# Optimization experiments

Measured on AMD Instinct MI355X. Metric: run time of the kernel, lower is better.

The kernel has to match this reference:

```python
import jax, jax.numpy as jnp
import numpy as np


def setup_inputs() -> dict:
    key = jax.random.key(0)
    ks = jax.random.split(key, 5)
    S, B, I, H = 512, 64, 256, 1024
    scale_x = 1.0 / np.sqrt(I)
    scale_h = 1.0 / np.sqrt(H)
    return {
        "x": jax.random.normal(ks[0], (S, B, I), dtype=jnp.float32),
        "Wx": jax.random.normal(ks[1], (H, I), dtype=jnp.float32) * scale_x,
        "bx": jax.random.normal(ks[2], (H,), dtype=jnp.float32) * scale_x,
        "Wh": jax.random.normal(ks[3], (H, H), dtype=jnp.float32) * scale_h,
        "bh": jax.random.normal(ks[4], (H,), dtype=jnp.float32) * scale_h,
    }


def reference(x, Wx, bx, Wh, bh):
    # x: (S, B, I). Vanilla RNN: h_t = tanh(Wh h_{t-1} + bh + Wx x_t + bx)
    S, B, I = x.shape
    H = Wh.shape[0]
    # Precompute input projections for all timesteps in one big GEMM.
    xproj = jnp.einsum("sbi,hi->sbh", x, Wx) + bx  # (S, B, H)

    def step(h, xp_t):
        h_new = jnp.tanh(h @ Wh.T + bh + xp_t)  # (B, H)
        return h_new, h_new

    h0 = jnp.zeros((B, H), dtype=x.dtype)
    h_last, h_seq = jax.lax.scan(step, h0, xproj)
    return h_seq, h_last[None]  # (S,B,H), (1,B,H)
```

## Files before the change

### kernel.cpp

```cpp
#include <hip/hip_runtime.h>
#include <cstddef>

#define S_ 512
#define B_ 64
#define I_ 256
#define H_ 1024

#define NG 8
#define GB 8
#define JT 32
#define GBLK 32

__global__ __launch_bounds__(256) void transpose_k(const float* __restrict__ in,
                                                   float* __restrict__ out,
                                                   int R, int C) {
  __shared__ float t[32][33];
  int c0 = blockIdx.x * 32, r0 = blockIdx.y * 32;
  int x = threadIdx.x & 31, y = threadIdx.x >> 5;
  for (int i = 0; i < 32; i += 8) {
    t[y + i][x] = in[(size_t)(r0 + y + i) * C + (c0 + x)];
  }
  __syncthreads();
  for (int i = 0; i < 32; i += 8) {
    out[(size_t)(c0 + y + i) * R + (r0 + x)] = t[x][y + i];
  }
}

__global__ __launch_bounds__(256) void xproj_kernel(const float* __restrict__ x,
                                                    const float* __restrict__ WxT,
                                                    const float* __restrict__ bx,
                                                    float* __restrict__ out) {
  __shared__ float xs[4][I_];
  int tid = threadIdx.x;
  int j = blockIdx.x * 256 + tid;
  size_t m0 = (size_t)blockIdx.y * 4;
  const float* xrow = x + m0 * I_;
  for (int r = 0; r < 4; ++r) xs[r][tid] = xrow[(size_t)r * I_ + tid];
  __syncthreads();

  float bj = bx[j];
  float a0 = bj, a1 = bj, a2 = bj, a3 = bj;
  const float* wp = WxT + j;
  for (int k = 0; k < I_; k += 4) {
    float w0 = wp[(size_t)(k + 0) * H_];
    float w1 = wp[(size_t)(k + 1) * H_];
    float w2 = wp[(size_t)(k + 2) * H_];
    float w3 = wp[(size_t)(k + 3) * H_];
    float4 v0 = *(const float4*)&xs[0][k];
    float4 v1 = *(const float4*)&xs[1][k];
    float4 v2 = *(const float4*)&xs[2][k];
    float4 v3 = *(const float4*)&xs[3][k];
    a0 += w0 * v0.x + w1 * v0.y + w2 * v0.z + w3 * v0.w;
    a1 += w0 * v1.x + w1 * v1.y + w2 * v1.z + w3 * v1.w;
    a2 += w0 * v2.x + w1 * v2.y + w2 * v2.z + w3 * v2.w;
    a3 += w0 * v3.x + w1 * v3.y + w2 * v3.z + w3 * v3.w;
  }
  out[(m0 + 0) * H_ + j] = a0;
  out[(m0 + 1) * H_ + j] = a1;
  out[(m0 + 2) * H_ + j] = a2;
  out[(m0 + 3) * H_ + j] = a3;
}

__global__ __launch_bounds__(256) void rnn_persistent(const float* __restrict__ Wh,
                                                      const float* __restrict__ bh,
                                                      float* __restrict__ out,
                                                      unsigned* __restrict__ bar) {
  __shared__ float4 Hs4[GB * 256];

  const int tid = threadIdx.x;
  const int g  = blockIdx.x & 7;
  const int jt = blockIdx.x >> 3;
  const int j0 = jt * JT, b0 = g * GB;
  const int jj = tid >> 3;
  const int ks = tid & 7;

  float4 Wreg[32];
  {
    const float4* wp = (const float4*)(Wh + (size_t)(j0 + jj) * H_) + ks * 32;
    #pragma unroll
    for (int i = 0; i < 32; ++i) Wreg[i] = wp[i];
  }
  const float bh_j = bh[j0 + jj];
  const size_t oidx = (size_t)(b0 + ks) * H_ + (size_t)(j0 + jj);
  float* const out_last = out + (size_t)S_ * B_ * H_;
  unsigned* const barg = bar + (size_t)g * 32;

  for (int t = 0; t < S_; ++t) {
    float* orow = out + (size_t)t * B_ * H_;
    float xv = orow[oidx];

    float s = 0.f;
    if (t > 0) {
      const float* hsrc =
          (const float*)(out + (size_t)(t - 1) * B_ * H_ + (size_t)b0 * H_);
      float4 hv[8];
      #pragma unroll
      for (int q = 0; q < 8; ++q) {
        const float* ap = hsrc + (size_t)(q * 256 + tid) * 4;
        asm volatile("global_load_dwordx4 %0, %1, off sc1"
                     : "=v"(hv[q]) : "v"(ap));
      }
      asm volatile("s_waitcnt vmcnt(0)" ::: "memory");
      __builtin_amdgcn_sched_barrier(0);
      #pragma unroll
      for (int q = 0; q < 8; ++q) {
        int idx = q * 256 + tid;
        Hs4[idx ^ ((idx >> 5) & 7)] = hv[q];
      }
      __syncthreads();

      float acc[8] = {0.f, 0.f, 0.f, 0.f, 0.f, 0.f, 0.f, 0.f};
      const int kb = ks * 32;
      #pragma unroll
      for (int i = 0; i < 32; ++i) {
        const float4 w = Wreg[i];
        const int l0 = (kb + i) ^ ks;
        #pragma unroll
        for (int b = 0; b < 8; ++b) {
          float4 h = Hs4[b * 256 + l0];
          acc[b] += w.x * h.x + w.y * h.y + w.z * h.z + w.w * h.w;
        }
      }
      #pragma unroll
      for (int b = 0; b < 8; ++b) {
        float v = acc[b];
        v += __shfl_xor(v, 1, 64);
        v += __shfl_xor(v, 2, 64);
        v += __shfl_xor(v, 4, 64);
        acc[b] = v;
      }
      float sv = acc[0];
      #pragma unroll
      for (int b = 1; b < 8; ++b) sv = (ks == b) ? acc[b] : sv;
      s = sv;
    }

    float hval = tanhf(s + bh_j + xv);
    if (t == S_ - 1) out_last[oidx] = hval;
    __hip_atomic_store(&orow[oidx], hval, __ATOMIC_RELAXED,
                       __HIP_MEMORY_SCOPE_AGENT);

    if (t < S_ - 1) {
      asm volatile("s_waitcnt vmcnt(0)" ::: "memory");
      __syncthreads();
      if (tid == 0) {
        __hip_atomic_fetch_add(barg, 1u, __ATOMIC_RELAXED,
                               __HIP_MEMORY_SCOPE_AGENT);
        const unsigned tgt = (unsigned)GBLK * (unsigned)(t + 1);
        while (__hip_atomic_load(barg, __ATOMIC_RELAXED,
                                 __HIP_MEMORY_SCOPE_AGENT) < tgt)
          __builtin_amdgcn_s_sleep(1);
      }
      __syncthreads();
    }
  }
}

extern "C" void kernel_launch(void* const* d_in, const int* in_sizes, int n_in,
                              void* d_out, int out_size, void* d_ws, size_t ws_size,
                              hipStream_t stream) {
  const float* x  = (const float*)d_in[0];
  const float* Wx = (const float*)d_in[1];
  const float* bx = (const float*)d_in[2];
  const float* Wh = (const float*)d_in[3];
  const float* bh = (const float*)d_in[4];
  float* out = (float*)d_out;
  float* WxT = (float*)d_ws;
  unsigned* bar = (unsigned*)(WxT + (size_t)I_ * H_);

  (void)hipMemsetAsync(bar, 0, NG * 32 * sizeof(unsigned), stream);
  hipLaunchKernelGGL(transpose_k, dim3(I_ / 32, H_ / 32), dim3(256), 0, stream,
                     Wx, WxT, H_, I_);
  hipLaunchKernelGGL(xproj_kernel, dim3(H_ / 256, (S_ * B_) / 4), dim3(256), 0, stream,
                     x, WxT, bx, out);

  void* args[] = {(void*)&Wh, (void*)&bh, (void*)&out, (void*)&bar};
  (void)hipLaunchCooperativeKernel((const void*)rnn_persistent, dim3(256),
                                   dim3(256), args, 0, stream);
}
```

Before: 4.494 ms.

## Use per-block step flags, double threads per block, and widen xproj row tiling

The group barrier drops the shared atomic counter that every block incremented. Each block now writes its own step flag, and 32 lanes poll all the flags in the group, which removes contention on one atomic. The persistent kernel goes to 512 threads, halving the per-thread K slice and the register-resident weights (16 float4 instead of 32) and adding one more shuffle stage. It keeps the swizzled LDS layout. The xproj kernel now processes 8 rows per block instead of 4, so each weight load is reused more. The costs are idle lanes during the tanh and store step, and more polling traffic.

Measured after the change: 4.295 ms. 1.05x faster.

```diff
diff --git a/kernel.cpp b/kernel.cpp
--- a/kernel.cpp
+++ b/kernel.cpp
@@ -30,60 +30,59 @@
                                                     const float* __restrict__ WxT,
                                                     const float* __restrict__ bx,
                                                     float* __restrict__ out) {
-  __shared__ float xs[4][I_];
+  __shared__ float xs[8][I_];
   int tid = threadIdx.x;
   int j = blockIdx.x * 256 + tid;
-  size_t m0 = (size_t)blockIdx.y * 4;
+  size_t m0 = (size_t)blockIdx.y * 8;
   const float* xrow = x + m0 * I_;
-  for (int r = 0; r < 4; ++r) xs[r][tid] = xrow[(size_t)r * I_ + tid];
+  #pragma unroll
+  for (int r = 0; r < 8; ++r) xs[r][tid] = xrow[(size_t)r * I_ + tid];
   __syncthreads();
 
   float bj = bx[j];
-  float a0 = bj, a1 = bj, a2 = bj, a3 = bj;
+  float a[8];
+  #pragma unroll
+  for (int r = 0; r < 8; ++r) a[r] = bj;
   const float* wp = WxT + j;
   for (int k = 0; k < I_; k += 4) {
     float w0 = wp[(size_t)(k + 0) * H_];
     float w1 = wp[(size_t)(k + 1) * H_];
     float w2 = wp[(size_t)(k + 2) * H_];
     float w3 = wp[(size_t)(k + 3) * H_];
-    float4 v0 = *(const float4*)&xs[0][k];
-    float4 v1 = *(const float4*)&xs[1][k];
-    float4 v2 = *(const float4*)&xs[2][k];
-    float4 v3 = *(const float4*)&xs[3][k];
-    a0 += w0 * v0.x + w1 * v0.y + w2 * v0.z + w3 * v0.w;
-    a1 += w0 * v1.x + w1 * v1.y + w2 * v1.z + w3 * v1.w;
-    a2 += w0 * v2.x + w1 * v2.y + w2 * v2.z + w3 * v2.w;
-    a3 += w0 * v3.x + w1 * v3.y + w2 * v3.z + w3 * v3.w;
+    #pragma unroll
+    for (int r = 0; r < 8; ++r) {
+      float4 v = *(const float4*)&xs[r][k];
+      a[r] += w0 * v.x + w1 * v.y + w2 * v.z + w3 * v.w;
+    }
   }
-  out[(m0 + 0) * H_ + j] = a0;
-  out[(m0 + 1) * H_ + j] = a1;
-  out[(m0 + 2) * H_ + j] = a2;
-  out[(m0 + 3) * H_ + j] = a3;
+  #pragma unroll
+  for (int r = 0; r < 8; ++r) out[(m0 + r) * H_ + j] = a[r];
 }
 
-__global__ __launch_bounds__(256) void rnn_persistent(const float* __restrict__ Wh,
+__global__ __launch_bounds__(512) void rnn_persistent(const float* __restrict__ Wh,
                                                       const float* __restrict__ bh,
                                                       float* __restrict__ out,
-                                                      unsigned* __restrict__ bar) {
+                                                      unsigned* __restrict__ flags) {
   __shared__ float4 Hs4[GB * 256];
 
   const int tid = threadIdx.x;
   const int g  = blockIdx.x & 7;
   const int jt = blockIdx.x >> 3;
   const int j0 = jt * JT, b0 = g * GB;
-  const int jj = tid >> 3;
-  const int ks = tid & 7;
+  const int jj = tid >> 4;
+  const int ks = tid & 15;
+  const int ksw = ks & 7;
 
-  float4 Wreg[32];
+  float4 Wreg[16];
   {
-    const float4* wp = (const float4*)(Wh + (size_t)(j0 + jj) * H_) + ks * 32;
+    const float4* wp = (const float4*)(Wh + (size_t)(j0 + jj) * H_) + ks * 16;
     #pragma unroll
-    for (int i = 0; i < 32; ++i) Wreg[i] = wp[i];
+    for (int i = 0; i < 16; ++i) Wreg[i] = wp[i];
   }
   const float bh_j = bh[j0 + jj];
-  const size_t oidx = (size_t)(b0 + ks) * H_ + (size_t)(j0 + jj);
+  const size_t oidx = (size_t)(b0 + ksw) * H_ + (size_t)(j0 + jj);
   float* const out_last = out + (size_t)S_ * B_ * H_;
-  unsigned* const barg = bar + (size_t)g * 32;
+  unsigned* const flagg = flags + (size_t)g * GBLK;
 
   for (int t = 0; t < S_; ++t) {
     float* orow = out + (size_t)t * B_ * H_;
@@ -93,28 +92,28 @@
     if (t > 0) {
       const float* hsrc =
           (const float*)(out + (size_t)(t - 1) * B_ * H_ + (size_t)b0 * H_);
-      float4 hv[8];
+      float4 hv[4];
       #pragma unroll
-      for (int q = 0; q < 8; ++q) {
-        const float* ap = hsrc + (size_t)(q * 256 + tid) * 4;
+      for (int q = 0; q < 4; ++q) {
+        const float* ap = hsrc + (size_t)(q * 512 + tid) * 4;
         asm volatile("global_load_dwordx4 %0, %1, off sc1"
                      : "=v"(hv[q]) : "v"(ap));
       }
       asm volatile("s_waitcnt vmcnt(0)" ::: "memory");
       __builtin_amdgcn_sched_barrier(0);
       #pragma unroll
-      for (int q = 0; q < 8; ++q) {
-        int idx = q * 256 + tid;
-        Hs4[idx ^ ((idx >> 5) & 7)] = hv[q];
+      for (int q = 0; q < 4; ++q) {
+        int f = q * 512 + tid;
+        Hs4[f ^ ((f >> 4) & 7)] = hv[q];
       }
       __syncthreads();
 
       float acc[8] = {0.f, 0.f, 0.f, 0.f, 0.f, 0.f, 0.f, 0.f};
-      const int kb = ks * 32;
+      const int kb = ks * 16;
       #pragma unroll
-      for (int i = 0; i < 32; ++i) {
+      for (int i = 0; i < 16; ++i) {
+        const int l0 = kb + (i ^ ksw);
         const float4 w = Wreg[i];
-        const int l0 = (kb + i) ^ ks;
         #pragma unroll
         for (int b = 0; b < 8; ++b) {
           float4 h = Hs4[b * 256 + l0];
@@ -127,6 +126,7 @@
         v += __shfl_xor(v, 1, 64);
         v += __shfl_xor(v, 2, 64);
         v += __shfl_xor(v, 4, 64);
+        v += __shfl_xor(v, 8, 64);
         acc[b] = v;
       }
       float sv = acc[0];
@@ -135,19 +135,24 @@
       s = sv;
     }
 
-    float hval = tanhf(s + bh_j + xv);
-    if (t == S_ - 1) out_last[oidx] = hval;
-    __hip_atomic_store(&orow[oidx], hval, __ATOMIC_RELAXED,
-                       __HIP_MEMORY_SCOPE_AGENT);
+    if (ks < GB) {
+      float hval = tanhf(s + bh_j + xv);
+      if (t == S_ - 1) out_last[oidx] = hval;
+      __hip_atomic_store(&orow[oidx], hval, __ATOMIC_RELAXED,
+                         __HIP_MEMORY_SCOPE_AGENT);
+    }
 
     if (t < S_ - 1) {
       asm volatile("s_waitcnt vmcnt(0)" ::: "memory");
       __syncthreads();
       if (tid == 0) {
-        __hip_atomic_fetch_add(barg, 1u, __ATOMIC_RELAXED,
-                               __HIP_MEMORY_SCOPE_AGENT);
-        const unsigned tgt = (unsigned)GBLK * (unsigned)(t + 1);
-        while (__hip_atomic_load(barg, __ATOMIC_RELAXED,
+        __hip_atomic_store(&flagg[jt], (unsigned)(t + 1), __ATOMIC_RELAXED,
+                           __HIP_MEMORY_SCOPE_AGENT);
+      }
+      if (tid < 64) {
+        unsigned* fp = &flagg[tid & 31];
+        const unsigned tgt = (unsigned)(t + 1);
+        while (__hip_atomic_load(fp, __ATOMIC_RELAXED,
                                  __HIP_MEMORY_SCOPE_AGENT) < tgt)
           __builtin_amdgcn_s_sleep(1);
       }
@@ -166,15 +171,19 @@
   const float* bh = (const float*)d_in[4];
   float* out = (float*)d_out;
   float* WxT = (float*)d_ws;
-  unsigned* bar = (unsigned*)(WxT + (size_t)I_ * H_);
+  unsigned* flags = (unsigned*)(WxT + (size_t)I_ * H_);
 
-  (void)hipMemsetAsync(bar, 0, NG * 32 * sizeof(unsigned), stream);
+  (void)hipMemsetAsync(flags, 0, NG * GBLK * sizeof(unsigned), stream);
   hipLaunchKernelGGL(transpose_k, dim3(I_ / 32, H_ / 32), dim3(256), 0, stream,
                      Wx, WxT, H_, I_);
-  hipLaunchKernelGGL(xproj_kernel, dim3(H_ / 256, (S_ * B_) / 4), dim3(256), 0, stream,
+  hipLaunchKernelGGL(xproj_kernel, dim3(H_ / 256, (S_ * B_) / 8), dim3(256), 0, stream,
                      x, WxT, bx, out);
 
-  void* args[] = {(void*)&Wh, (void*)&bh, (void*)&out, (void*)&bar};
-  (void)hipLaunchCooperativeKernel((const void*)rnn_persistent, dim3(256),
-                                   dim3(256), args, 0, stream);
+  void* args[] = {(void*)&Wh, (void*)&bh, (void*)&out, (void*)&flags};
+  hipError_t e = hipLaunchCooperativeKernel((const void*)rnn_persistent,
+                                            dim3(256), dim3(512), args, 0, stream);
+  if (e != hipSuccess) {
+    hipLaunchKernelGGL(rnn_persistent, dim3(256), dim3(512), 0, stream,
+                       Wh, bh, out, flags);
+  }
 }
```
